# Kernel optimization log

Hardware: AMD Instinct MI355X
Metric: run time of the kernel (lower is better)

## Reference

```python
import jax, jax.numpy as jnp
import numpy as np

MAX_ANTS = 16  # padded max draws per (batch, neuron); ragged draws masked with -1
BS, N_IN, N_OUT = 32, 4096, 4096


def setup_inputs() -> dict:
    key = jax.random.key(0)
    k1, k2 = jax.random.split(key)
    # integer ant counts per (batch, input neuron), in [0, MAX_ANTS)
    x = jax.random.randint(k1, (BS, N_IN), 0, MAX_ANTS, dtype=jnp.int32)
    # positive weights (original init is uniform 1/n_outputs; random positive is general)
    weights = jax.random.uniform(k2, (N_IN, N_OUT), dtype=jnp.float32, minval=0.01, maxval=1.0)
    return {"x": x, "weights": weights}


def reference(x, weights):
    """Vectorized equivalent of ACOLayer.forward.

    Original: for each batch b and input neuron i with count c = x[b, i] > 0,
    draw c iid categorical samples from row-normalized weights[i].
    Here: inverse-CDF sampling, padded to MAX_ANTS draws, invalid slots = -1.
    Returns int32 [bs, n_in, MAX_ANTS].
    """
    probs = weights / weights.sum(axis=1, keepdims=True)   # normalize()
    cdf = jnp.cumsum(probs, axis=1)                        # [n_in, n_out]
    bs, n_in = x.shape
    n_out = weights.shape[1]
    u = jax.random.uniform(jax.random.key(42), (bs, n_in, MAX_ANTS), dtype=weights.dtype)
    # group draws by input neuron so each row's CDF is searched once
    u_rows = u.transpose(1, 0, 2).reshape(n_in, bs * MAX_ANTS)  # [n_in, bs*MAX]
    idx = jax.vmap(jnp.searchsorted)(cdf, u_rows)               # inverse-CDF draw
    idx = jnp.minimum(idx, n_out - 1).astype(jnp.int32)
    idx = idx.reshape(n_in, bs, MAX_ANTS).transpose(1, 0, 2)    # [bs, n_in, MAX]
    valid = jnp.arange(MAX_ANTS, dtype=x.dtype)[None, None, :] < x[:, :, None]
    return jnp.where(valid, idx, -1)
```

## Files before the change

kernel.cpp:

```cpp
#include <hip/hip_runtime.h>
#include <stdint.h>


#define N_IN   4096
#define N_OUT  4096
#define BS     32
#define MAX_A  16
#define THREADS 256
#define HALF   1048576u

__device__ __forceinline__ int padi(int j) { return j + ((j >> 6) << 2); }

__device__ __forceinline__ uint32_t rotl32(uint32_t x, uint32_t r) {
    return (x << r) | (x >> (32u - r));
}

__device__ __forceinline__ void threefry2x32_42(uint32_t x0, uint32_t x1,
                                                uint32_t& o0, uint32_t& o1) {
    const uint32_t k0 = 0u, k1 = 42u;
    const uint32_t k2 = k0 ^ k1 ^ 0x1BD11BDAu;
    x0 += k0; x1 += k1;
#define TF_R(r) { x0 += x1; x1 = rotl32(x1, (r)); x1 ^= x0; }
    TF_R(13) TF_R(15) TF_R(26) TF_R(6)
    x0 += k1; x1 += k2 + 1u;
    TF_R(17) TF_R(29) TF_R(16) TF_R(24)
    x0 += k2; x1 += k0 + 2u;
    TF_R(13) TF_R(15) TF_R(26) TF_R(6)
    x0 += k0; x1 += k1 + 3u;
    TF_R(17) TF_R(29) TF_R(16) TF_R(24)
    x0 += k1; x1 += k2 + 4u;
    TF_R(13) TF_R(15) TF_R(26) TF_R(6)
    x0 += k2; x1 += k0 + 5u;
#undef TF_R
    o0 = x0; o1 = x1;
}

__device__ __forceinline__ float bits_to_uniform(uint32_t b) {
    uint32_t f = (b >> 9) | 0x3f800000u;
    float r;
    __builtin_memcpy(&r, &f, 4);
    return r - 1.0f;
}

__device__ __forceinline__ int lower_bound_cdf(const float* cdf, float tval) {
    int lo = 0, hi = N_OUT;
    #pragma unroll
    for (int it = 0; it < 12; ++it) {
        int mid = (lo + hi) >> 1;
        if (cdf[padi(mid)] < tval) lo = mid + 1; else hi = mid;
    }
    return lo < N_OUT ? lo : N_OUT - 1;
}

__global__ __launch_bounds__(THREADS)
void aco_sample_kernel(const int* __restrict__ x,
                       const float* __restrict__ w,
                       int* __restrict__ out) {
    __shared__ float cdf[N_OUT + (N_OUT >> 4)];
    __shared__ float wsum[4];
    __shared__ int   xc[BS];

    const int row  = blockIdx.x;
    const int t    = threadIdx.x;
    const int lane = t & 63;
    const int wid  = t >> 6;

    const float4* wrow = (const float4*)(w + (size_t)row * N_OUT);
    float4 v0 = wrow[t * 4 + 0];
    float4 v1 = wrow[t * 4 + 1];
    float4 v2 = wrow[t * 4 + 2];
    float4 v3 = wrow[t * 4 + 3];

    if (t < BS) xc[t] = x[t * N_IN + row];

    float loc[16];
    {
        float s = 0.f;
        s += v0.x; loc[0]  = s;  s += v0.y; loc[1]  = s;
        s += v0.z; loc[2]  = s;  s += v0.w; loc[3]  = s;
        s += v1.x; loc[4]  = s;  s += v1.y; loc[5]  = s;
        s += v1.z; loc[6]  = s;  s += v1.w; loc[7]  = s;
        s += v2.x; loc[8]  = s;  s += v2.y; loc[9]  = s;
        s += v2.z; loc[10] = s;  s += v2.w; loc[11] = s;
        s += v3.x; loc[12] = s;  s += v3.y; loc[13] = s;
        s += v3.z; loc[14] = s;  s += v3.w; loc[15] = s;
    }
    const float my_total = loc[15];

    float incl = my_total;
    #pragma unroll
    for (int d = 1; d < 64; d <<= 1) {
        float n = __shfl_up(incl, d, 64);
        if (lane >= d) incl += n;
    }
    if (lane == 63) wsum[wid] = incl;
    __syncthreads();

    const float4 ws = *(const float4*)wsum;
    const float total = ws.x + ws.y + ws.z + ws.w;
    float wprefix = 0.f;
    if (wid > 0) wprefix += ws.x;
    if (wid > 1) wprefix += ws.y;
    if (wid > 2) wprefix += ws.z;
    const float chunk_prefix = wprefix + incl - my_total;

    float* cbase = &cdf[padi(t * 16)];
    {
        float4 a, b, c, d;
        a.x = chunk_prefix + loc[0];  a.y = chunk_prefix + loc[1];
        a.z = chunk_prefix + loc[2];  a.w = chunk_prefix + loc[3];
        b.x = chunk_prefix + loc[4];  b.y = chunk_prefix + loc[5];
        b.z = chunk_prefix + loc[6];  b.w = chunk_prefix + loc[7];
        c.x = chunk_prefix + loc[8];  c.y = chunk_prefix + loc[9];
        c.z = chunk_prefix + loc[10]; c.w = chunk_prefix + loc[11];
        d.x = chunk_prefix + loc[12]; d.y = chunk_prefix + loc[13];
        d.z = chunk_prefix + loc[14]; d.w = chunk_prefix + loc[15];
        ((float4*)cbase)[0] = a;
        ((float4*)cbase)[1] = b;
        ((float4*)cbase)[2] = c;
        ((float4*)cbase)[3] = d;
    }
    __syncthreads();

    const int b = t >> 4;
    const int a = t & 15;
    const uint32_t j0 = (uint32_t)(b * (N_IN * MAX_A) + row * MAX_A + a);
    const uint32_t j1 = j0 + HALF;

    uint32_t o0, o1, p0, p1;
    threefry2x32_42(0u, j0, o0, o1);
    threefry2x32_42(0u, j1, p0, p1);
    const float t0 = bits_to_uniform(o0 ^ o1) * total;
    const float t1 = bits_to_uniform(p0 ^ p1) * total;

    const int idx0 = lower_bound_cdf(cdf, t0);
    const int idx1 = lower_bound_cdf(cdf, t1);

    out[j0] = (a < xc[b])      ? idx0 : -1;
    out[j1] = (a < xc[b + 16]) ? idx1 : -1;
}

extern "C" void kernel_launch(void* const* d_in, const int* in_sizes, int n_in,
                              void* d_out, int out_size, void* d_ws, size_t ws_size,
                              hipStream_t stream) {
    const int*   x;
    const float* w;
    if (in_sizes[0] == BS * N_IN) { x = (const int*)d_in[0]; w = (const float*)d_in[1]; }
    else                          { x = (const int*)d_in[1]; w = (const float*)d_in[0]; }
    aco_sample_kernel<<<N_IN, THREADS, 0, stream>>>(x, w, (int*)d_out);
}
```

Baseline: 21.35 us.

## Use bucketed CDF lookup table to narrow binary search range

Builds a 512-entry bucket table in shared memory that maps each uniform-value bucket to the first CDF index reaching that bucket. Each draw then binary-searches only within its bucket's index range instead of performing 12 full LDS probes. This adds a table-building pass, an extra barrier, and a variable-trip loop with divergence. Bucket rounding near boundaries could produce off-by-one index differences.

```diff
diff --git a/kernel.cpp b/kernel.cpp
--- a/kernel.cpp
+++ b/kernel.cpp
@@ -2,12 +2,13 @@
 #include <stdint.h>
 
 
-#define N_IN   4096
-#define N_OUT  4096
-#define BS     32
-#define MAX_A  16
+#define N_IN    4096
+#define N_OUT   4096
+#define BS      32
+#define MAX_A   16
 #define THREADS 256
-#define HALF   1048576u
+#define HALF    1048576u
+#define BUCKETS 512
 
 __device__ __forceinline__ int padi(int j) { return j + ((j >> 6) << 2); }
 
@@ -42,21 +43,12 @@
     return r - 1.0f;
 }
 
-__device__ __forceinline__ int lower_bound_cdf(const float* cdf, float tval) {
-    int lo = 0, hi = N_OUT;
-    #pragma unroll
-    for (int it = 0; it < 12; ++it) {
-        int mid = (lo + hi) >> 1;
-        if (cdf[padi(mid)] < tval) lo = mid + 1; else hi = mid;
-    }
-    return lo < N_OUT ? lo : N_OUT - 1;
-}
-
 __global__ __launch_bounds__(THREADS)
 void aco_sample_kernel(const int* __restrict__ x,
                        const float* __restrict__ w,
                        int* __restrict__ out) {
     __shared__ float cdf[N_OUT + (N_OUT >> 4)];
+    __shared__ int   btab[BUCKETS + 1];
     __shared__ float wsum[4];
     __shared__ int   xc[BS];
 
@@ -72,6 +64,9 @@
     float4 v3 = wrow[t * 4 + 3];
 
     if (t < BS) xc[t] = x[t * N_IN + row];
+    btab[t]       = N_OUT - 1;
+    btab[t + 256] = N_OUT - 1;
+    if (t == 0) btab[BUCKETS] = N_OUT - 1;
 
     float loc[16];
     {
@@ -122,6 +117,19 @@
     }
     __syncthreads();
 
+    const float scale = (float)BUCKETS / total;
+    int kprev;
+    if (t == 0) kprev = -1;
+    else        kprev = (int)(cdf[padi(t * 16 - 1)] * scale);
+    #pragma unroll
+    for (int m = 0; m < 16; ++m) {
+        int kj = (int)((chunk_prefix + loc[m]) * scale);
+        if (kj > BUCKETS) kj = BUCKETS;
+        for (int b2 = kprev + 1; b2 <= kj; ++b2) btab[b2] = t * 16 + m;
+        kprev = kj;
+    }
+    __syncthreads();
+
     const int b = t >> 4;
     const int a = t & 15;
     const uint32_t j0 = (uint32_t)(b * (N_IN * MAX_A) + row * MAX_A + a);
@@ -130,14 +138,29 @@
     uint32_t o0, o1, p0, p1;
     threefry2x32_42(0u, j0, o0, o1);
     threefry2x32_42(0u, j1, p0, p1);
-    const float t0 = bits_to_uniform(o0 ^ o1) * total;
-    const float t1 = bits_to_uniform(p0 ^ p1) * total;
+    const float u0 = bits_to_uniform(o0 ^ o1);
+    const float u1 = bits_to_uniform(p0 ^ p1);
+    const float t0 = u0 * total;
+    const float t1 = u1 * total;
+    const int   k0 = (int)(u0 * (float)BUCKETS);
+    const int   k1 = (int)(u1 * (float)BUCKETS);
 
-    const int idx0 = lower_bound_cdf(cdf, t0);
-    const int idx1 = lower_bound_cdf(cdf, t1);
+    int lo0 = btab[k0], hi0 = btab[k0 + 1];
+    int lo1 = btab[k1], hi1 = btab[k1 + 1];
 
-    out[j0] = (a < xc[b])      ? idx0 : -1;
-    out[j1] = (a < xc[b + 16]) ? idx1 : -1;
+    while (lo0 < hi0 || lo1 < hi1) {
+        if (lo0 < hi0) {
+            int m = (lo0 + hi0) >> 1;
+            if (cdf[padi(m)] < t0) lo0 = m + 1; else hi0 = m;
+        }
+        if (lo1 < hi1) {
+            int m = (lo1 + hi1) >> 1;
+            if (cdf[padi(m)] < t1) lo1 = m + 1; else hi1 = m;
+        }
+    }
+
+    out[j0] = (a < xc[b])      ? lo0 : -1;
+    out[j1] = (a < xc[b + 16]) ? lo1 : -1;
 }
 
 extern "C" void kernel_launch(void* const* d_in, const int* in_sizes, int n_in,
```

New measurement: 24.17 us. 1.13x slower.

## Process two rows per block, prefetching second row during first search

Applied to the files above, without the earlier changes.

Each block now handles two input rows, and the grid is halved to match. The second row's weight loads and its RNG draws are issued before the binary searches on the first row's CDF, so global memory latency can overlap with shared-memory search work. The shared CDF buffer is reused, with barriers separating the two phases. In exchange there are fewer, longer blocks, which may reduce latency hiding across waves, and there are extra synchronizations and higher register pressure from the prefetched float4s.

```diff
diff --git a/kernel.cpp b/kernel.cpp
--- a/kernel.cpp
+++ b/kernel.cpp
@@ -2,12 +2,13 @@
 #include <stdint.h>
 
 
-#define N_IN   4096
-#define N_OUT  4096
-#define BS     32
-#define MAX_A  16
+#define N_IN    4096
+#define N_OUT   4096
+#define BS      32
+#define MAX_A   16
 #define THREADS 256
-#define HALF   1048576u
+#define HALF    1048576u
+#define GRID    (N_IN / 2)
 
 __device__ __forceinline__ int padi(int j) { return j + ((j >> 6) << 2); }
 
@@ -52,41 +53,66 @@
     return lo < N_OUT ? lo : N_OUT - 1;
 }
 
+__device__ __forceinline__ float local_scan16(const float4& v0, const float4& v1,
+                                              const float4& v2, const float4& v3,
+                                              float* loc) {
+    float s = 0.f;
+    s += v0.x; loc[0]  = s;  s += v0.y; loc[1]  = s;
+    s += v0.z; loc[2]  = s;  s += v0.w; loc[3]  = s;
+    s += v1.x; loc[4]  = s;  s += v1.y; loc[5]  = s;
+    s += v1.z; loc[6]  = s;  s += v1.w; loc[7]  = s;
+    s += v2.x; loc[8]  = s;  s += v2.y; loc[9]  = s;
+    s += v2.z; loc[10] = s;  s += v2.w; loc[11] = s;
+    s += v3.x; loc[12] = s;  s += v3.y; loc[13] = s;
+    s += v3.z; loc[14] = s;  s += v3.w; loc[15] = s;
+    return s;
+}
+
+__device__ __forceinline__ void write_cdf16(float* cbase, const float* loc, float pfx) {
+    float4 a, b, c, d;
+    a.x = pfx + loc[0];  a.y = pfx + loc[1];  a.z = pfx + loc[2];  a.w = pfx + loc[3];
+    b.x = pfx + loc[4];  b.y = pfx + loc[5];  b.z = pfx + loc[6];  b.w = pfx + loc[7];
+    c.x = pfx + loc[8];  c.y = pfx + loc[9];  c.z = pfx + loc[10]; c.w = pfx + loc[11];
+    d.x = pfx + loc[12]; d.y = pfx + loc[13]; d.z = pfx + loc[14]; d.w = pfx + loc[15];
+    ((float4*)cbase)[0] = a;
+    ((float4*)cbase)[1] = b;
+    ((float4*)cbase)[2] = c;
+    ((float4*)cbase)[3] = d;
+}
+
 __global__ __launch_bounds__(THREADS)
 void aco_sample_kernel(const int* __restrict__ x,
                        const float* __restrict__ w,
                        int* __restrict__ out) {
     __shared__ float cdf[N_OUT + (N_OUT >> 4)];
     __shared__ float wsum[4];
-    __shared__ int   xc[BS];
+    __shared__ int   xc[2][BS];
 
-    const int row  = blockIdx.x;
     const int t    = threadIdx.x;
     const int lane = t & 63;
     const int wid  = t >> 6;
+    const int row0 = blockIdx.x;
+    const int row1 = blockIdx.x + GRID;
 
-    const float4* wrow = (const float4*)(w + (size_t)row * N_OUT);
-    float4 v0 = wrow[t * 4 + 0];
-    float4 v1 = wrow[t * 4 + 1];
-    float4 v2 = wrow[t * 4 + 2];
-    float4 v3 = wrow[t * 4 + 3];
+    const float4* wr0 = (const float4*)(w + (size_t)row0 * N_OUT);
+    float4 a0 = wr0[t * 4 + 0];
+    float4 a1 = wr0[t * 4 + 1];
+    float4 a2 = wr0[t * 4 + 2];
+    float4 a3 = wr0[t * 4 + 3];
+    if (t < BS)           xc[0][t]      = x[t * N_IN + row0];
+    else if (t < 2 * BS)  xc[1][t - BS] = x[(t - BS) * N_IN + row1];
 
-    if (t < BS) xc[t] = x[t * N_IN + row];
+    const int bb = t >> 4;
+    const int aa = t & 15;
+    const uint32_t jA = (uint32_t)(bb * (N_IN * MAX_A) + row0 * MAX_A + aa);
+    uint32_t o0, o1, p0, p1;
+    threefry2x32_42(0u, jA, o0, o1);
+    threefry2x32_42(0u, jA + HALF, p0, p1);
+    const float uA0 = bits_to_uniform(o0 ^ o1);
+    const float uA1 = bits_to_uniform(p0 ^ p1);
 
     float loc[16];
-    {
-        float s = 0.f;
-        s += v0.x; loc[0]  = s;  s += v0.y; loc[1]  = s;
-        s += v0.z; loc[2]  = s;  s += v0.w; loc[3]  = s;
-        s += v1.x; loc[4]  = s;  s += v1.y; loc[5]  = s;
-        s += v1.z; loc[6]  = s;  s += v1.w; loc[7]  = s;
-        s += v2.x; loc[8]  = s;  s += v2.y; loc[9]  = s;
-        s += v2.z; loc[10] = s;  s += v2.w; loc[11] = s;
-        s += v3.x; loc[12] = s;  s += v3.y; loc[13] = s;
-        s += v3.z; loc[14] = s;  s += v3.w; loc[15] = s;
-    }
-    const float my_total = loc[15];
-
+    float my_total = local_scan16(a0, a1, a2, a3, loc);
     float incl = my_total;
     #pragma unroll
     for (int d = 1; d < 64; d <<= 1) {
@@ -96,48 +122,62 @@
     if (lane == 63) wsum[wid] = incl;
     __syncthreads();
 
-    const float4 ws = *(const float4*)wsum;
-    const float total = ws.x + ws.y + ws.z + ws.w;
-    float wprefix = 0.f;
-    if (wid > 0) wprefix += ws.x;
-    if (wid > 1) wprefix += ws.y;
-    if (wid > 2) wprefix += ws.z;
-    const float chunk_prefix = wprefix + incl - my_total;
-
-    float* cbase = &cdf[padi(t * 16)];
+    float4 ws = *(const float4*)wsum;
+    const float totalA = ws.x + ws.y + ws.z + ws.w;
     {
-        float4 a, b, c, d;
-        a.x = chunk_prefix + loc[0];  a.y = chunk_prefix + loc[1];
-        a.z = chunk_prefix + loc[2];  a.w = chunk_prefix + loc[3];
-        b.x = chunk_prefix + loc[4];  b.y = chunk_prefix + loc[5];
-        b.z = chunk_prefix + loc[6];  b.w = chunk_prefix + loc[7];
-        c.x = chunk_prefix + loc[8];  c.y = chunk_prefix + loc[9];
-        c.z = chunk_prefix + loc[10]; c.w = chunk_prefix + loc[11];
-        d.x = chunk_prefix + loc[12]; d.y = chunk_prefix + loc[13];
-        d.z = chunk_prefix + loc[14]; d.w = chunk_prefix + loc[15];
-        ((float4*)cbase)[0] = a;
-        ((float4*)cbase)[1] = b;
-        ((float4*)cbase)[2] = c;
-        ((float4*)cbase)[3] = d;
+        float wprefix = 0.f;
+        if (wid > 0) wprefix += ws.x;
+        if (wid > 1) wprefix += ws.y;
+        if (wid > 2) wprefix += ws.z;
+        write_cdf16(&cdf[padi(t * 16)], loc, wprefix + incl - my_total);
     }
     __syncthreads();
 
-    const int b = t >> 4;
-    const int a = t & 15;
-    const uint32_t j0 = (uint32_t)(b * (N_IN * MAX_A) + row * MAX_A + a);
-    const uint32_t j1 = j0 + HALF;
+    const float4* wr1 = (const float4*)(w + (size_t)row1 * N_OUT);
+    float4 b0 = wr1[t * 4 + 0];
+    float4 b1 = wr1[t * 4 + 1];
+    float4 b2 = wr1[t * 4 + 2];
+    float4 b3 = wr1[t * 4 + 3];
+    const uint32_t jB = (uint32_t)(bb * (N_IN * MAX_A) + row1 * MAX_A + aa);
+    threefry2x32_42(0u, jB, o0, o1);
+    threefry2x32_42(0u, jB + HALF, p0, p1);
+    const float uB0 = bits_to_uniform(o0 ^ o1);
+    const float uB1 = bits_to_uniform(p0 ^ p1);
 
-    uint32_t o0, o1, p0, p1;
-    threefry2x32_42(0u, j0, o0, o1);
-    threefry2x32_42(0u, j1, p0, p1);
-    const float t0 = bits_to_uniform(o0 ^ o1) * total;
-    const float t1 = bits_to_uniform(p0 ^ p1) * total;
+    {
+        const int idx0 = lower_bound_cdf(cdf, uA0 * totalA);
+        const int idx1 = lower_bound_cdf(cdf, uA1 * totalA);
+        out[jA]        = (aa < xc[0][bb])      ? idx0 : -1;
+        out[jA + HALF] = (aa < xc[0][bb + 16]) ? idx1 : -1;
+    }
 
-    const int idx0 = lower_bound_cdf(cdf, t0);
-    const int idx1 = lower_bound_cdf(cdf, t1);
+    my_total = local_scan16(b0, b1, b2, b3, loc);
+    incl = my_total;
+    #pragma unroll
+    for (int d = 1; d < 64; d <<= 1) {
+        float n = __shfl_up(incl, d, 64);
+        if (lane >= d) incl += n;
+    }
+    if (lane == 63) wsum[wid] = incl;
+    __syncthreads();
 
-    out[j0] = (a < xc[b])      ? idx0 : -1;
-    out[j1] = (a < xc[b + 16]) ? idx1 : -1;
+    ws = *(const float4*)wsum;
+    const float totalB = ws.x + ws.y + ws.z + ws.w;
+    {
+        float wprefix = 0.f;
+        if (wid > 0) wprefix += ws.x;
+        if (wid > 1) wprefix += ws.y;
+        if (wid > 2) wprefix += ws.z;
+        write_cdf16(&cdf[padi(t * 16)], loc, wprefix + incl - my_total);
+    }
+    __syncthreads();
+
+    {
+        const int idx0 = lower_bound_cdf(cdf, uB0 * totalB);
+        const int idx1 = lower_bound_cdf(cdf, uB1 * totalB);
+        out[jB]        = (aa < xc[1][bb])      ? idx0 : -1;
+        out[jB + HALF] = (aa < xc[1][bb + 16]) ? idx1 : -1;
+    }
 }
 
 extern "C" void kernel_launch(void* const* d_in, const int* in_sizes, int n_in,
@@ -147,5 +187,5 @@
     const float* w;
     if (in_sizes[0] == BS * N_IN) { x = (const int*)d_in[0]; w = (const float*)d_in[1]; }
     else                          { x = (const int*)d_in[1]; w = (const float*)d_in[0]; }
-    aco_sample_kernel<<<N_IN, THREADS, 0, stream>>>(x, w, (int*)d_out);
+    aco_sample_kernel<<<GRID, THREADS, 0, stream>>>(x, w, (int*)d_out);
 }
```

Result: slower. 24.20 us (+13.4%).
